# Optimization experiments

Hardware: AMD Instinct MI355X
Metric: run time of the kernel (lower is better)

The kernel has to match this reference:

```python
import jax, jax.numpy as jnp
from jax import lax
import numpy as np

BN_EPS = 1e-5


def conv_transpose2d(x, w, b, stride, pad):
    # torch ConvTranspose2d weight layout: (in, out, kH, kW)
    k = w.shape[2]
    wt = jnp.flip(w, (2, 3)).transpose(1, 0, 2, 3)  # (out, in, kH, kW)
    p = k - 1 - pad
    out = lax.conv_general_dilated(
        x, wt, window_strides=(1, 1), padding=[(p, p), (p, p)],
        lhs_dilation=(stride, stride),
        dimension_numbers=("NCHW", "OIHW", "NCHW"))
    return out + b[None, :, None, None]


def conv2d(x, w, b, pad):
    out = lax.conv_general_dilated(
        x, w, window_strides=(1, 1), padding=[(pad, pad), (pad, pad)],
        dimension_numbers=("NCHW", "OIHW", "NCHW"))
    return out + b[None, :, None, None]


def batchnorm2d(x, gamma, beta):
    # training-mode BN: batch statistics over (N, H, W), biased variance
    mean = jnp.mean(x, axis=(0, 2, 3), keepdims=True)
    var = jnp.mean((x - mean) ** 2, axis=(0, 2, 3), keepdims=True)
    xn = (x - mean) * lax.rsqrt(var + BN_EPS)
    return xn * gamma[None, :, None, None] + beta[None, :, None, None]


def setup_inputs():
    key = jax.random.key(0)
    ks = jax.random.split(key, 8)
    B = 4096
    return {
        "x": jax.random.randint(ks[0], (B,), 0, 60032, dtype=jnp.int32),
        "encoder_w": jax.random.normal(ks[1], (60032, 7 * 7 * 64), jnp.float32) * 0.02,
        "emb_w": jax.random.normal(ks[2], (512, 64), jnp.float32) * 0.02,
        "deconv1_w": jax.random.normal(ks[3], (64, 32, 4, 4), jnp.float32) * 0.03,
        "deconv1_b": jnp.zeros((32,), jnp.float32),
        "bn1_g": jnp.ones((32,), jnp.float32),
        "bn1_b": jnp.zeros((32,), jnp.float32),
        "deconv2_w": jax.random.normal(ks[4], (32, 16, 4, 4), jnp.float32) * 0.04,
        "deconv2_b": jnp.zeros((16,), jnp.float32),
        "bn2_g": jnp.ones((16,), jnp.float32),
        "bn2_b": jnp.zeros((16,), jnp.float32),
        "conv_w": jax.random.normal(ks[5], (1, 16, 3, 3), jnp.float32) * 0.08,
        "conv_b": jnp.zeros((1,), jnp.float32),
    }


def reference(x, encoder_w, emb_w, deconv1_w, deconv1_b, bn1_g, bn1_b,
              deconv2_w, deconv2_b, bn2_g, bn2_b, conv_w, conv_b):
    # encoder embedding lookup -> [B, 64, 7, 7]
    z_e_x = encoder_w[x].reshape(-1, 64, 7, 7)
    z = z_e_x.transpose(0, 2, 3, 1)  # [B, H, W, C]
    # squared L2 distances to codebook, computed without the [B,H,W,C,K] blowup:
    # ||z||^2 - 2 z.e + ||e||^2, identical math to the broadcast-pow-sum
    d = ((z ** 2).sum(-1, keepdims=True)
         - 2.0 * jnp.einsum("bhwc,kc->bhwk", z, emb_w)
         + (emb_w ** 2).sum(-1))  # [B, H, W, K]
    latents = jnp.argmin(d, axis=-1)  # [B, H, W]
    z_q_x = emb_w[latents].transpose(0, 3, 1, 2)  # [B, 64, 7, 7]
    # decoder
    h = jax.nn.relu(batchnorm2d(conv_transpose2d(z_q_x, deconv1_w, deconv1_b, 2, 1), bn1_g, bn1_b))
    h = jax.nn.relu(batchnorm2d(conv_transpose2d(h, deconv2_w, deconv2_b, 2, 1), bn2_g, bn2_b))
    x_tilde = jax.nn.sigmoid(conv2d(h, conv_w, conv_b, 1))  # [B, 1, 28, 28]
    return (x_tilde, z_e_x, z_q_x)
```

## Files before the change

### kernel.cpp

```cpp
#include <hip/hip_runtime.h>
#include <hip/hip_bf16.h>
#include <math.h>

#define BATCH   4096
#define CH      64
#define KCB     512

#define XT_N    (BATCH*784)
#define ZE_OFF  (XT_N)
#define ZQ_OFF  (XT_N + BATCH*3136)

#define WS_C1   0
#define WS_C2   51380224ULL
#define WS_ST   154140672ULL
#define WS_WF2  154141824ULL
#define WS_EF   154158208ULL
#define WS_EE   154289280ULL
#define WS_WF1  WS_C2

typedef __attribute__((ext_vector_type(8))) __bf16 bf16x8;
typedef __attribute__((ext_vector_type(4))) float f32x4;
union B8 { uint4 u; bf16x8 v; };

__device__ inline unsigned short f2bf(float f) {
    unsigned int u = __float_as_uint(f);
    u = u + 0x7fffu + ((u >> 16) & 1u);
    return (unsigned short)(u >> 16);
}
__device__ inline float bf2f(unsigned short h) {
    return __uint_as_float(((unsigned int)h) << 16);
}

__global__ void k_prep(const float* __restrict__ w1, const float* __restrict__ w2,
                       const float* __restrict__ emb,
                       unsigned short* __restrict__ w1f, unsigned short* __restrict__ w2f,
                       unsigned short* __restrict__ ef, float* __restrict__ eeW,
                       double* __restrict__ stats) {
    int t = threadIdx.x + blockIdx.x * 256;
    if (t < 96) stats[t] = 0.0;
    {
        int i = t & 7, lane = (t >> 3) & 63, frag = t >> 9;
        int mt = frag >> 2, khalf = (frag >> 1) & 1, hilo = frag & 1;
        int cw = mt * 16 + (lane & 15);
        int k  = khalf * 32 + ((lane >> 4) << 3) + i;
        float v = emb[(cw << 6) + k];
        unsigned short h = f2bf(v);
        ef[t] = hilo ? f2bf(v - bf2f(h)) : h;
    }
    if (t < 32768) {
        int i = t & 7, lane = (t >> 3) & 63, frag = t >> 9;
        int cls = frag >> 4, tap = (frag >> 2) & 3, khalf = (frag >> 1) & 1, mt = frag & 1;
        int ph = cls >> 1, pw = cls & 1, dh = tap >> 1, dw = tap & 1;
        int kh = (1 - ph) + 2 * dh, kw = (1 - pw) + 2 * dw;
        int oc = mt * 16 + (lane & 15);
        int ic = khalf * 32 + ((lane >> 4) << 3) + i;
        w1f[t] = f2bf(w1[((ic * 32 + oc) << 4) + kh * 4 + kw]);
    }
    if (t < 8192) {
        int i = t & 7, lane = (t >> 3) & 63, frag = t >> 9;
        int cls = frag >> 2, tap = frag & 3;
        int ph = cls >> 1, pw = cls & 1, dh = tap >> 1, dw = tap & 1;
        int kh = (1 - ph) + 2 * dh, kw = (1 - pw) + 2 * dw;
        int oc = lane & 15;
        int ic = ((lane >> 4) << 3) + i;
        w2f[t] = f2bf(w2[((ic * 16 + oc) << 4) + kh * 4 + kw]);
    }
    if (t < KCB) {
        double s = 0.0;
        const float* e = emb + (t << 6);
        for (int c = 0; c < CH; ++c) s += (double)e[c] * (double)e[c];
        eeW[t] = (float)s;
    }
}

__global__ __launch_bounds__(256) void k1_encode(
    const int* __restrict__ xidx, const float* __restrict__ encW,
    const float* __restrict__ emb, const unsigned short* __restrict__ ef,
    const float* __restrict__ eeW, float* __restrict__ out)
{
    __shared__ __align__(16) unsigned short zh_s[128*72];
    __shared__ __align__(16) unsigned short zl_s[128*72];
    __shared__ float ee_s[KCB];
    __shared__ float zzp[128][2];

    const int tid = threadIdx.x, wave = tid >> 6, lane = tid & 63;
    const int blk = blockIdx.x;

    for (int k = tid; k < KCB; k += 256) ee_s[k] = eeW[k];

    {
        const int pos = tid & 127, h = tid >> 7;
        float zacc = 0.f;
        const int p  = blk*128 + pos;
        const int b  = p / 49;
        const int hw = p - b*49;
        const long long row = xidx[b];
        const float* rp = encW + row*3136LL + hw;
        float* zep = out + ZE_OFF + (long long)b*3136 + hw;
        #pragma unroll
        for (int j = 0; j < 32; ++j) {
            int c = h + 2*j;
            float v = rp[c*49];
            zep[c*49] = v;
            unsigned short hb = f2bf(v);
            float r = v - bf2f(hb);
            zh_s[pos*72 + c] = hb;
            zl_s[pos*72 + c] = f2bf(r);
            zacc = fmaf(v, v, zacc);
        }
        zzp[pos][h] = zacc;
    }
    __syncthreads();

    const int col = lane & 15, g = lane >> 4;
    B8 Bh[2][2], Bl[2][2];
    #pragma unroll
    for (int t2 = 0; t2 < 2; ++t2) {
        int pos = (wave*2 + t2)*16 + col;
        #pragma unroll
        for (int kh = 0; kh < 2; ++kh) {
            Bh[t2][kh].u = *(const uint4*)(zh_s + pos*72 + kh*32 + g*8);
            Bl[t2][kh].u = *(const uint4*)(zl_s + pos*72 + kh*32 + g*8);
        }
    }

    float d0[2] = {3.4e38f, 3.4e38f}, d1[2] = {3.4e38f, 3.4e38f};
    int   k0[2] = {0, 0},             k1i[2] = {1, 1};

    const uint4* ap = (const uint4*)ef + lane;
    uint4 A0 = ap[0*64], A1 = ap[1*64], A2 = ap[2*64], A3 = ap[3*64];

    for (int mt = 0; mt < 32; ++mt) {
        B8 Ah0, Al0, Ah1, Al1;
        Ah0.u = A0; Al0.u = A1; Ah1.u = A2; Al1.u = A3;
        if (mt < 31) {
            const uint4* np = ap + (mt+1)*256;
            A0 = np[0]; A1 = np[64]; A2 = np[128]; A3 = np[192];
        }
        const float4 eev = *(const float4*)&ee_s[mt*16 + (g << 2)];
        #pragma unroll
        for (int t2 = 0; t2 < 2; ++t2) {
            f32x4 acc = {eev.x*-0.5f, eev.y*-0.5f, eev.z*-0.5f, eev.w*-0.5f};
            acc = __builtin_amdgcn_mfma_f32_16x16x32_bf16(Ah0.v, Bh[t2][0].v, acc, 0,0,0);
            acc = __builtin_amdgcn_mfma_f32_16x16x32_bf16(Ah1.v, Bh[t2][1].v, acc, 0,0,0);
            acc = __builtin_amdgcn_mfma_f32_16x16x32_bf16(Ah0.v, Bl[t2][0].v, acc, 0,0,0);
            acc = __builtin_amdgcn_mfma_f32_16x16x32_bf16(Ah1.v, Bl[t2][1].v, acc, 0,0,0);
            acc = __builtin_amdgcn_mfma_f32_16x16x32_bf16(Al0.v, Bh[t2][0].v, acc, 0,0,0);
            acc = __builtin_amdgcn_mfma_f32_16x16x32_bf16(Al1.v, Bh[t2][1].v, acc, 0,0,0);
            #pragma unroll
            for (int rg = 0; rg < 4; ++rg) {
                float s = -2.f * acc[rg];
                int  cw = mt*16 + (g << 2) + rg;
                if (s < d0[t2] || (s == d0[t2] && cw < k0[t2])) {
                    d1[t2] = d0[t2]; k1i[t2] = k0[t2]; d0[t2] = s; k0[t2] = cw;
                } else if (s < d1[t2] || (s == d1[t2] && cw < k1i[t2])) {
                    d1[t2] = s; k1i[t2] = cw;
                }
            }
        }
    }

    #pragma unroll
    for (int t2 = 0; t2 < 2; ++t2) {
        #pragma unroll
        for (int msk = 16; msk <= 32; msk <<= 1) {
            float e0 = __shfl_xor(d0[t2], msk), e1 = __shfl_xor(d1[t2], msk);
            int   j0 = __shfl_xor(k0[t2], msk), j1 = __shfl_xor(k1i[t2], msk);
            if (e0 < d0[t2] || (e0 == d0[t2] && j0 < k0[t2])) {
                if (d0[t2] < e1 || (d0[t2] == e1 && k0[t2] < j1)) { d1[t2] = d0[t2]; k1i[t2] = k0[t2]; }
                else                                              { d1[t2] = e1;     k1i[t2] = j1;     }
                d0[t2] = e0; k0[t2] = j0;
            } else {
                if (e0 < d1[t2] || (e0 == d1[t2] && j0 < k1i[t2])) { d1[t2] = e0; k1i[t2] = j0; }
            }
        }

        const int pos = (wave*2 + t2)*16 + col;
        const int p   = blk*128 + pos;
        const int b   = p / 49;
        const int hw  = p - b*49;
        const float zz = zzp[pos][0] + zzp[pos][1];
        int win = k0[t2];

        if (d1[t2] - d0[t2] < fmaxf(1e-6f, 1e-3f * fabsf(d0[t2] + zz))) {
            const float* zp = out + ZE_OFF + (long long)b*3136 + hw;
            const float* ea = emb + k0[t2]*CH;
            const float* eb = emb + k1i[t2]*CH;
            double D0 = 0.0, D1 = 0.0;
            for (int c = 0; c < CH; ++c) {
                double zv = (double)zp[c*49];
                double f0 = zv - (double)ea[c];
                double f1 = zv - (double)eb[c];
                D0 += f0*f0; D1 += f1*f1;
            }
            if (D1 < D0 || (D1 == D0 && k1i[t2] < k0[t2])) win = k1i[t2];
        }

        float* zqp = out + ZQ_OFF + (long long)b*3136 + hw;
        const float* e0p = emb + win*CH + g*16;
        #pragma unroll
        for (int j = 0; j < 16; ++j) zqp[(g*16 + j)*49] = e0p[j];
    }
}

__global__ __launch_bounds__(256) void k2_deconv1(
    const float* __restrict__ zq, const unsigned short* __restrict__ w1f,
    const float* __restrict__ b1, unsigned short* __restrict__ c1cls,
    double* __restrict__ stats)
{
    __shared__ __align__(16) unsigned short x_s[2*81*72];
    __shared__ float bs[32], bq[32];

    const int tid = threadIdx.x, wave = tid >> 6, lane = tid & 63;
    const int b0 = blockIdx.x << 1;

    for (int i = tid; i < 2*81*72/2; i += 256) ((unsigned int*)x_s)[i] = 0u;
    if (tid < 32) { bs[tid] = 0.f; bq[tid] = 0.f; }
    __syncthreads();

    for (int i = tid; i < 6272; i += 256) {
        int img = i >= 3136;
        int e = i - img*3136;
        int c = e / 49, hw = e - c*49;
        int ih = hw / 7, iw = hw - ih*7;
        float v = zq[(long long)(b0+img)*3136 + e];
        x_s[img*5832 + ((ih+1)*9 + (iw+1))*72 + c] = f2bf(v);
    }
    __syncthreads();

    const int cls = wave, ph = cls >> 1, pw = cls & 1;
    bf16x8 wfr[4][2][2];
    {
        const uint4* wp = (const uint4*)w1f + (cls*16)*64 + lane;
        #pragma unroll
        for (int tap = 0; tap < 4; ++tap)
            #pragma unroll
            for (int kh2 = 0; kh2 < 2; ++kh2)
                #pragma unroll
                for (int mt = 0; mt < 2; ++mt) {
                    B8 t; t.u = wp[(tap*4 + kh2*2 + mt)*64];
                    wfr[tap][kh2][mt] = t.v;
                }
    }
    float biasv[2][4];
    #pragma unroll
    for (int mt = 0; mt < 2; ++mt)
        #pragma unroll
        for (int rg = 0; rg < 4; ++rg)
            biasv[mt][rg] = b1[mt*16 + ((lane >> 4) << 2) + rg];

    float ts[2][4] = {{0.f}}, tq[2][4] = {{0.f}};
    const int gb = (lane >> 4) << 4;

    for (int nt = 0; nt < 7; ++nt) {
        int m = nt*16 + (lane & 15);
        bool valid = m < 98;
        int mm = valid ? m : 0;
        int img = mm >= 49;
        int px = mm - img*49;
        int a = px / 7, bb = px - a*7;
        f32x4 acc0 = {0.f,0.f,0.f,0.f}, acc1 = {0.f,0.f,0.f,0.f};
        #pragma unroll
        for (int dh = 0; dh < 2; ++dh)
            #pragma unroll
            for (int dw = 0; dw < 2; ++dw) {
                int tap = dh*2 + dw;
                int r = (a + ph - dh + 1)*9 + (bb + pw - dw + 1);
                const char* p = (const char*)x_s + img*11664 + r*144 + gb;
                B8 x0; x0.u = *(const uint4*)p;
                B8 x1; x1.u = *(const uint4*)(p + 64);
                acc0 = __builtin_amdgcn_mfma_f32_16x16x32_bf16(wfr[tap][0][0], x0.v, acc0, 0,0,0);
                acc1 = __builtin_amdgcn_mfma_f32_16x16x32_bf16(wfr[tap][0][1], x0.v, acc1, 0,0,0);
                acc0 = __builtin_amdgcn_mfma_f32_16x16x32_bf16(wfr[tap][1][0], x1.v, acc0, 0,0,0);
                acc1 = __builtin_amdgcn_mfma_f32_16x16x32_bf16(wfr[tap][1][1], x1.v, acc1, 0,0,0);
            }
        if (valid) {
            unsigned short* base = c1cls + (long long)(b0+img)*6272 + cls*1568 + px;
            #pragma unroll
            for (int rg = 0; rg < 4; ++rg) {
                int oc = ((lane >> 4) << 2) + rg;
                float v0 = acc0[rg] + biasv[0][rg];
                float v1 = acc1[rg] + biasv[1][rg];
                base[oc*49]      = f2bf(v0);
                base[(oc+16)*49] = f2bf(v1);
                ts[0][rg] += v0; tq[0][rg] = fmaf(v0, v0, tq[0][rg]);
                ts[1][rg] += v1; tq[1][rg] = fmaf(v1, v1, tq[1][rg]);
            }
        }
    }

    #pragma unroll
    for (int mt = 0; mt < 2; ++mt)
        #pragma unroll
        for (int rg = 0; rg < 4; ++rg) {
            float s = ts[mt][rg], q = tq[mt][rg];
            #pragma unroll
            for (int msk = 1; msk < 16; msk <<= 1) {
                s += __shfl_xor(s, msk);
                q += __shfl_xor(q, msk);
            }
            if ((lane & 15) == 0) {
                int oc = mt*16 + ((lane >> 4) << 2) + rg;
                atomicAdd(&bs[oc], s);
                atomicAdd(&bq[oc], q);
            }
        }
    __syncthreads();
    if (tid < 32) {
        atomicAdd(&stats[tid],      (double)bs[tid]);
        atomicAdd(&stats[32 + tid], (double)bq[tid]);
    }
}

__global__ __launch_bounds__(256) void k4_deconv2(
    const unsigned short* __restrict__ c1cls, const unsigned short* __restrict__ w2f,
    const float* __restrict__ b2, const float* __restrict__ g1,
    const float* __restrict__ be1, double* stats,
    unsigned short* __restrict__ c2cls)
{
    __shared__ __align__(16) unsigned short x_s[256*40];
    __shared__ float bnl[64];
    __shared__ float bs[16], bq[16];

    const int tid = threadIdx.x, wave = tid >> 6, lane = tid & 63;
    const int b = blockIdx.x;

    for (int i = tid; i < 256*40/2; i += 256) ((unsigned int*)x_s)[i] = 0u;
    if (tid < 32) {
        const double n = 4096.0*196.0;
        double mean = stats[tid] / n;
        double var  = stats[32 + tid] / n - mean*mean;
        double rstd = 1.0 / sqrt(var + 1e-5);
        double sc   = (double)g1[tid] * rstd;
        bnl[tid]      = (float)sc;
        bnl[32 + tid] = (float)((double)be1[tid] - mean*sc);
    }
    if (tid < 16) { bs[tid] = 0.f; bq[tid] = 0.f; }
    __syncthreads();

    const unsigned short* cb = c1cls + (long long)b*6272;
    for (int i = tid; i < 6272; i += 256) {
        int cl = i / 1568, e = i - cl*1568;
        int ic = e / 49, pxc = e - ic*49;
        int a = pxc / 7, bb = pxc - a*7;
        int ih = 2*a + (cl >> 1), iw = 2*bb + (cl & 1);
        float v = fmaxf(fmaf(bf2f(cb[i]), bnl[ic], bnl[32 + ic]), 0.f);
        x_s[((ih+1)*16 + (iw+1))*40 + ic] = f2bf(v);
    }
    __syncthreads();

    const int cls = wave, ph = cls >> 1, pw = cls & 1;
    bf16x8 wfr[4];
    {
        const uint4* wp = (const uint4*)w2f + (cls*4)*64 + lane;
        #pragma unroll
        for (int tap = 0; tap < 4; ++tap) { B8 t; t.u = wp[tap*64]; wfr[tap] = t.v; }
    }
    float biasv[4];
    #pragma unroll
    for (int rg = 0; rg < 4; ++rg) biasv[rg] = b2[((lane >> 4) << 2) + rg];

    float ts[4] = {0.f}, tq[4] = {0.f};
    unsigned short* c2b = c2cls + (long long)b*12544 + cls*3136;
    const int gb = (lane >> 4) << 4;

    for (int nt = 0; nt < 13; ++nt) {
        int m = nt*16 + (lane & 15);
        bool valid = m < 196;
        int px = valid ? m : 0;
        int a = px / 14, bb = px - a*14;
        f32x4 acc = {0.f,0.f,0.f,0.f};
        #pragma unroll
        for (int dh = 0; dh < 2; ++dh)
            #pragma unroll
            for (int dw = 0; dw < 2; ++dw) {
                int tap = dh*2 + dw;
                int r = (a + ph - dh + 1)*16 + (bb + pw - dw + 1);
                B8 x0; x0.u = *(const uint4*)((const char*)x_s + r*80 + gb);
                acc = __builtin_amdgcn_mfma_f32_16x16x32_bf16(wfr[tap], x0.v, acc, 0,0,0);
            }
        if (valid) {
            unsigned short* base = c2b + px;
            #pragma unroll
            for (int rg = 0; rg < 4; ++rg) {
                int oc = ((lane >> 4) << 2) + rg;
                float v = acc[rg] + biasv[rg];
                base[oc*196] = f2bf(v);
                ts[rg] += v; tq[rg] = fmaf(v, v, tq[rg]);
            }
        }
    }

    #pragma unroll
    for (int rg = 0; rg < 4; ++rg) {
        float s = ts[rg], q = tq[rg];
        #pragma unroll
        for (int msk = 1; msk < 16; msk <<= 1) {
            s += __shfl_xor(s, msk);
            q += __shfl_xor(q, msk);
        }
        if ((lane & 15) == 0) {
            int oc = ((lane >> 4) << 2) + rg;
            atomicAdd(&bs[oc], s);
            atomicAdd(&bq[oc], q);
        }
    }
    __syncthreads();
    if (tid < 16) {
        atomicAdd(&stats[64 + tid], (double)bs[tid]);
        atomicAdd(&stats[80 + tid], (double)bq[tid]);
    }
}

__global__ __launch_bounds__(256) void k6_conv(
    const unsigned short* __restrict__ c2cls, const float* __restrict__ cw,
    const float* __restrict__ cbias, const float* __restrict__ g2,
    const float* __restrict__ be2, const double* __restrict__ stats,
    float* __restrict__ out)
{
    __shared__ float x_s[9*31*16];
    __shared__ float w_s[144];
    __shared__ float bn2[32];

    const int tid  = threadIdx.x;
    const int b    = blockIdx.x >> 2;
    const int qrt  = blockIdx.x & 3;
    const int r0   = qrt*7 - 1;

    for (int i = tid; i < 9*31*16; i += 256) x_s[i] = 0.f;
    if (tid < 144) {
        int ic = tid / 9, khw = tid - ic*9;
        w_s[khw*16 + ic] = cw[tid];
    }
    if (tid >= 192 && tid < 208) {
        int c = tid - 192;
        const double n = 4096.0*784.0;
        double mean = stats[64 + c] / n;
        double var  = stats[80 + c] / n - mean*mean;
        double rstd = 1.0 / sqrt(var + 1e-5);
        double sc   = (double)g2[c] * rstd;
        bn2[c]      = (float)sc;
        bn2[16 + c] = (float)((double)be2[c] - mean*sc);
    }
    __syncthreads();

    const unsigned short* cr = c2cls + (long long)b*12544;
    for (int i = tid; i < 4032; i += 256) {
        int c = i / 252, rem = i - c*252;
        int rr = rem / 28, iw = rem - rr*28;
        int ih = r0 + rr;
        if ((unsigned)ih < 28u) {
            int cl  = ((ih & 1) << 1) | (iw & 1);
            int px2 = (ih >> 1)*14 + (iw >> 1);
            float v = fmaxf(fmaf(bf2f(cr[cl*3136 + c*196 + px2]), bn2[c], bn2[16 + c]), 0.f);
            x_s[(rr*31 + (iw+1))*16 + c] = v;
        }
    }
    __syncthreads();

    const float bias = cbias[0];
    const int px = tid;
    if (px < 196) {
        int ohl = px / 28, ow = px - ohl*28;
        float a0=0.f,a1=0.f,a2=0.f,a3=0.f;
        #pragma unroll
        for (int kh = 0; kh < 3; ++kh) {
            #pragma unroll
            for (int kw = 0; kw < 3; ++kw) {
                const float4* xv = (const float4*)&x_s[((ohl+kh)*31 + ow+kw)*16];
                const float4* wv = (const float4*)&w_s[((kh*3 + kw) << 4)];
                #pragma unroll
                for (int c4 = 0; c4 < 4; ++c4) {
                    float4 xx = xv[c4];
                    float4 ww = wv[c4];
                    a0 = fmaf(xx.x, ww.x, a0);
                    a1 = fmaf(xx.y, ww.y, a1);
                    a2 = fmaf(xx.z, ww.z, a2);
                    a3 = fmaf(xx.w, ww.w, a3);
                }
            }
        }
        float t = ((a0+a1) + (a2+a3)) + bias;
        out[(long long)b*784 + (qrt*7 + ohl)*28 + ow] = 1.f / (1.f + expf(-t));
    }
}

extern "C" void kernel_launch(void* const* d_in, const int* in_sizes, int n_in,
                              void* d_out, int out_size, void* d_ws, size_t ws_size,
                              hipStream_t stream) {
    const int*   x    = (const int*)d_in[0];
    const float* encW = (const float*)d_in[1];
    const float* emb  = (const float*)d_in[2];
    const float* w1   = (const float*)d_in[3];
    const float* b1   = (const float*)d_in[4];
    const float* g1   = (const float*)d_in[5];
    const float* be1  = (const float*)d_in[6];
    const float* w2   = (const float*)d_in[7];
    const float* b2   = (const float*)d_in[8];
    const float* g2   = (const float*)d_in[9];
    const float* be2  = (const float*)d_in[10];
    const float* cw   = (const float*)d_in[11];
    const float* cb   = (const float*)d_in[12];
    float* out = (float*)d_out;

    char* ws = (char*)d_ws;
    unsigned short* c1cls = (unsigned short*)(ws + WS_C1);
    unsigned short* c2cls = (unsigned short*)(ws + WS_C2);
    double*         stats = (double*)(ws + WS_ST);
    unsigned short* w1f   = (unsigned short*)(ws + WS_WF1);
    unsigned short* w2f   = (unsigned short*)(ws + WS_WF2);
    unsigned short* ef    = (unsigned short*)(ws + WS_EF);
    float*          eeW   = (float*)(ws + WS_EE);

    k_prep<<<256, 256, 0, stream>>>(w1, w2, emb, w1f, w2f, ef, eeW, stats);
    k1_encode<<<1568, 256, 0, stream>>>(x, encW, emb, ef, eeW, out);
    k2_deconv1<<<2048, 256, 0, stream>>>(out + ZQ_OFF, w1f, b1, c1cls, stats);
    k4_deconv2<<<4096, 256, 0, stream>>>(c1cls, w2f, b2, g1, be1, stats, c2cls);
    k6_conv<<<16384, 256, 0, stream>>>(c2cls, cw, cb, g2, be2, stats, out);
}
```

Measured before the change: 465.3 us.

## Load encoder rows as contiguous float4 per image pair in encode kernel

The encode kernel now handles two images per block and reads each gathered encoder row as contiguous float4 loads, instead of strided per-channel scalar loads. The transposed bf16 split is scattered into shared memory instead. It adds the low×low MFMA terms so distances are more exact. The near-tie fallback now uses a fixed absolute threshold, and the z-norm accumulation is dropped. Each block computes 128 positions but only 98 are valid, so about a quarter of the MFMA work is wasted, and the grid grows to 2048 blocks.

```diff
diff --git a/kernel.cpp b/kernel.cpp
--- a/kernel.cpp
+++ b/kernel.cpp
@@ -78,37 +78,37 @@
     const float* __restrict__ emb, const unsigned short* __restrict__ ef,
     const float* __restrict__ eeW, float* __restrict__ out)
 {
-    __shared__ __align__(16) unsigned short zh_s[128*72];
-    __shared__ __align__(16) unsigned short zl_s[128*72];
+    __shared__ __align__(16) unsigned short zh_s[98*72];
+    __shared__ __align__(16) unsigned short zl_s[98*72];
     __shared__ float ee_s[KCB];
-    __shared__ float zzp[128][2];
 
     const int tid = threadIdx.x, wave = tid >> 6, lane = tid & 63;
-    const int blk = blockIdx.x;
+    const int b0 = blockIdx.x << 1;
 
     for (int k = tid; k < KCB; k += 256) ee_s[k] = eeW[k];
 
     {
-        const int pos = tid & 127, h = tid >> 7;
-        float zacc = 0.f;
-        const int p  = blk*128 + pos;
-        const int b  = p / 49;
-        const int hw = p - b*49;
-        const long long row = xidx[b];
-        const float* rp = encW + row*3136LL + hw;
-        float* zep = out + ZE_OFF + (long long)b*3136 + hw;
-        #pragma unroll
-        for (int j = 0; j < 32; ++j) {
-            int c = h + 2*j;
-            float v = rp[c*49];
-            zep[c*49] = v;
-            unsigned short hb = f2bf(v);
-            float r = v - bf2f(hb);
-            zh_s[pos*72 + c] = hb;
-            zl_s[pos*72 + c] = f2bf(r);
-            zacc = fmaf(v, v, zacc);
-        }
-        zzp[pos][h] = zacc;
+        const long long r0 = xidx[b0], r1 = xidx[b0 + 1];
+        const float4* src0 = (const float4*)(encW + r0*3136);
+        const float4* src1 = (const float4*)(encW + r1*3136);
+        float4* ze = (float4*)(out + ZE_OFF + (long long)b0*3136);
+        for (int i = tid; i < 1568; i += 256) {
+            float4 v = (i < 784) ? src0[i] : src1[i - 784];
+            ze[i] = v;
+            float vv[4] = {v.x, v.y, v.z, v.w};
+            int base = i << 2;
+            #pragma unroll
+            for (int j = 0; j < 4; ++j) {
+                int idx = base + j;
+                int img = idx >= 3136;
+                int e   = idx - img*3136;
+                int c   = e / 49, hw = e - c*49;
+                int pos = img*49 + hw;
+                unsigned short hb = f2bf(vv[j]);
+                zh_s[pos*72 + c] = hb;
+                zl_s[pos*72 + c] = f2bf(vv[j] - bf2f(hb));
+            }
+        }
     }
     __syncthreads();
 
@@ -116,11 +116,12 @@
     B8 Bh[2][2], Bl[2][2];
     #pragma unroll
     for (int t2 = 0; t2 < 2; ++t2) {
-        int pos = (wave*2 + t2)*16 + col;
+        int pos  = (wave*2 + t2)*16 + col;
+        int posc = pos < 98 ? pos : 97;
         #pragma unroll
         for (int kh = 0; kh < 2; ++kh) {
-            Bh[t2][kh].u = *(const uint4*)(zh_s + pos*72 + kh*32 + g*8);
-            Bl[t2][kh].u = *(const uint4*)(zl_s + pos*72 + kh*32 + g*8);
+            Bh[t2][kh].u = *(const uint4*)(zh_s + posc*72 + kh*32 + g*8);
+            Bl[t2][kh].u = *(const uint4*)(zl_s + posc*72 + kh*32 + g*8);
         }
     }
 
@@ -147,6 +148,8 @@
             acc = __builtin_amdgcn_mfma_f32_16x16x32_bf16(Ah1.v, Bl[t2][1].v, acc, 0,0,0);
             acc = __builtin_amdgcn_mfma_f32_16x16x32_bf16(Al0.v, Bh[t2][0].v, acc, 0,0,0);
             acc = __builtin_amdgcn_mfma_f32_16x16x32_bf16(Al1.v, Bh[t2][1].v, acc, 0,0,0);
+            acc = __builtin_amdgcn_mfma_f32_16x16x32_bf16(Al0.v, Bl[t2][0].v, acc, 0,0,0);
+            acc = __builtin_amdgcn_mfma_f32_16x16x32_bf16(Al1.v, Bl[t2][1].v, acc, 0,0,0);
             #pragma unroll
             for (int rg = 0; rg < 4; ++rg) {
                 float s = -2.f * acc[rg];
@@ -176,30 +179,31 @@
         }
 
         const int pos = (wave*2 + t2)*16 + col;
-        const int p   = blk*128 + pos;
-        const int b   = p / 49;
-        const int hw  = p - b*49;
-        const float zz = zzp[pos][0] + zzp[pos][1];
-        int win = k0[t2];
-
-        if (d1[t2] - d0[t2] < fmaxf(1e-6f, 1e-3f * fabsf(d0[t2] + zz))) {
-            const float* zp = out + ZE_OFF + (long long)b*3136 + hw;
-            const float* ea = emb + k0[t2]*CH;
-            const float* eb = emb + k1i[t2]*CH;
-            double D0 = 0.0, D1 = 0.0;
-            for (int c = 0; c < CH; ++c) {
-                double zv = (double)zp[c*49];
-                double f0 = zv - (double)ea[c];
-                double f1 = zv - (double)eb[c];
-                D0 += f0*f0; D1 += f1*f1;
-            }
-            if (D1 < D0 || (D1 == D0 && k1i[t2] < k0[t2])) win = k1i[t2];
-        }
-
-        float* zqp = out + ZQ_OFF + (long long)b*3136 + hw;
-        const float* e0p = emb + win*CH + g*16;
-        #pragma unroll
-        for (int j = 0; j < 16; ++j) zqp[(g*16 + j)*49] = e0p[j];
+        if (pos < 98) {
+            const int img = pos >= 49;
+            const int b   = b0 + img;
+            const int hw  = pos - img*49;
+            int win = k0[t2];
+
+            if (d1[t2] - d0[t2] < 5e-6f) {
+                const float* zp = out + ZE_OFF + (long long)b*3136 + hw;
+                const float* ea = emb + k0[t2]*CH;
+                const float* eb = emb + k1i[t2]*CH;
+                double D0 = 0.0, D1 = 0.0;
+                for (int c = 0; c < CH; ++c) {
+                    double zv = (double)zp[c*49];
+                    double f0 = zv - (double)ea[c];
+                    double f1 = zv - (double)eb[c];
+                    D0 += f0*f0; D1 += f1*f1;
+                }
+                if (D1 < D0 || (D1 == D0 && k1i[t2] < k0[t2])) win = k1i[t2];
+            }
+
+            float* zqp = out + ZQ_OFF + (long long)b*3136 + hw;
+            const float* e0p = emb + win*CH + g*16;
+            #pragma unroll
+            for (int j = 0; j < 16; ++j) zqp[(g*16 + j)*49] = e0p[j];
+        }
     }
 }
 
@@ -513,7 +517,7 @@
     float*          eeW   = (float*)(ws + WS_EE);
 
     k_prep<<<256, 256, 0, stream>>>(w1, w2, emb, w1f, w2f, ef, eeW, stats);
-    k1_encode<<<1568, 256, 0, stream>>>(x, encW, emb, ef, eeW, out);
+    k1_encode<<<2048, 256, 0, stream>>>(x, encW, emb, ef, eeW, out);
     k2_deconv1<<<2048, 256, 0, stream>>>(out + ZQ_OFF, w1f, b1, c1cls, stats);
     k4_deconv2<<<4096, 256, 0, stream>>>(c1cls, w2f, b2, g1, be1, stats, c2cls);
     k6_conv<<<16384, 256, 0, stream>>>(c2cls, cw, cb, g2, be2, stats, out);
```

Measured after the change: 472.7 us. About the same (+1.6%).
